# Kernel optimization log

Hardware: AMD Instinct MI355X
Metric: run time of the kernel (lower is better)

## Reference

```python
import jax, jax.numpy as jnp
import numpy as np

DIM, HEADS, HEAD_DIM = 1024, 16, 64
B, L, S = 4, 2048, 2048
EPS = 1e-5
NEG_INF = -1e9


def rms_norm(x, w):
    # x: [..., d]; normalize over last dim, scale by learned weight w [d]
    var = jnp.mean(jnp.square(x), axis=-1, keepdims=True)
    return x * jax.lax.rsqrt(var + EPS) * w


def setup_inputs() -> dict:
    key = jax.random.key(0)
    ks = jax.random.split(key, 9)
    hd = HEADS * HEAD_DIM
    scale = 1.0 / np.sqrt(DIM)
    return {
        "q": jax.random.normal(ks[0], (B, L, DIM), dtype=jnp.float32),
        "kv": jax.random.normal(ks[1], (B, S, DIM), dtype=jnp.float32),
        "x_seqlens": jax.random.randint(ks[2], (B,), 1, S + 1, dtype=jnp.int32),
        "Wq": jax.random.normal(ks[3], (DIM, hd), dtype=jnp.float32) * scale,
        "Wk": jax.random.normal(ks[4], (DIM, hd), dtype=jnp.float32) * scale,
        "Wv": jax.random.normal(ks[5], (DIM, hd), dtype=jnp.float32) * scale,
        "Wo": jax.random.normal(ks[6], (hd, DIM), dtype=jnp.float32) * (1.0 / np.sqrt(hd)),
        "q_norm_w": jnp.ones((HEAD_DIM,), dtype=jnp.float32),
        "k_norm_w": jnp.ones((HEAD_DIM,), dtype=jnp.float32),
    }


def reference(q, kv, x_seqlens, Wq, Wk, Wv, Wo, q_norm_w, k_norm_w):
    b, l, _ = q.shape
    s = kv.shape[1]
    # QKV projections -> [b, h, n, d]
    qh = (q @ Wq).reshape(b, l, HEADS, HEAD_DIM).transpose(0, 2, 1, 3)
    kh = (kv @ Wk).reshape(b, s, HEADS, HEAD_DIM).transpose(0, 2, 1, 3)
    vh = (kv @ Wv).reshape(b, s, HEADS, HEAD_DIM).transpose(0, 2, 1, 3)
    # per-head RMSNorm on q and k
    qh = rms_norm(qh, q_norm_w)
    kh = rms_norm(kh, k_norm_w)
    # dense padding mask [b, 1, 1, s]: True where kv position is valid
    mask = (jnp.arange(s, dtype=jnp.int32)[None, :] < x_seqlens[:, None])[:, None, None, :]
    # scaled dot-product attention (math path: full score matrix)
    scores = jnp.einsum("bhld,bhsd->bhls", qh, kh) * (1.0 / np.sqrt(HEAD_DIM))
    scores = jnp.where(mask, scores, NEG_INF)
    attn = jax.nn.softmax(scores, axis=-1)
    o = jnp.einsum("bhls,bhsd->bhld", attn, vh)  # [b, h, l, d]
    o = o.transpose(0, 2, 1, 3).reshape(b, l, HEADS * HEAD_DIM)
    return o @ Wo
```

## Files before the change

### kernel.cpp

```cpp
#include <hip/hip_runtime.h>
#include <hip/hip_bf16.h>
#include <stdint.h>

#define BB 4
#define LL 2048
#define SS 2048
#define DIMM 1024
#define HH 16
#define HD 64
#define NHD 1024

typedef __bf16 bf16_t;
typedef __bf16 bf16x8 __attribute__((ext_vector_type(8)));
typedef __bf16 bf16x4 __attribute__((ext_vector_type(4)));
typedef float f32x4 __attribute__((ext_vector_type(4)));

#define GLDS16(g, l) __builtin_amdgcn_global_load_lds( \
    (const __attribute__((address_space(1))) void*)(g), \
    (__attribute__((address_space(3))) void*)(l), 16, 0, 0)

#define FENCED_BARRIER() do {                    \
    asm volatile("" ::: "memory");               \
    __builtin_amdgcn_s_barrier();                \
    asm volatile("" ::: "memory");               \
    __builtin_amdgcn_sched_barrier(0);           \
  } while (0)

__global__ __launch_bounds__(256) void cvt_bf16(const float* __restrict__ in,
                                                bf16_t* __restrict__ out) {
  size_t i = (size_t)(blockIdx.x * 256 + threadIdx.x) * 8;
  const f32x4* p = (const f32x4*)(in + i);
  f32x4 a = p[0], b = p[1];
  bf16x8 o;
#pragma unroll
  for (int j = 0; j < 4; ++j) { o[j] = (bf16_t)a[j]; o[4 + j] = (bf16_t)b[j]; }
  *(bf16x8*)(out + i) = o;
}

__global__ __launch_bounds__(256) void transpose_cvt(const float* __restrict__ in,
                                                     bf16_t* __restrict__ out) {
  __shared__ float tile[64][65];
  const int r0 = blockIdx.y * 64, c0 = blockIdx.x * 64;
  const int tr = threadIdx.x >> 2;
  const int tc4 = (threadIdx.x & 3) * 16;
#pragma unroll
  for (int i = 0; i < 4; ++i) {
    f32x4 v = *(const f32x4*)&in[(size_t)(r0 + tr) * 1024 + c0 + tc4 + i * 4];
    tile[tr][tc4 + i * 4 + 0] = v.x;
    tile[tr][tc4 + i * 4 + 1] = v.y;
    tile[tr][tc4 + i * 4 + 2] = v.z;
    tile[tr][tc4 + i * 4 + 3] = v.w;
  }
  __syncthreads();
#pragma unroll
  for (int i = 0; i < 2; ++i) {
    bf16x8 o;
#pragma unroll
    for (int j = 0; j < 8; ++j) o[j] = (bf16_t)tile[tc4 + i * 8 + j][tr];
    *(bf16x8*)&out[(size_t)(c0 + tr) * 1024 + r0 + tc4 + i * 8] = o;
  }
}

template <int NORM, int OUTMODE>
__global__ __launch_bounds__(256) void gemm128(const bf16_t* __restrict__ A,
                                               const bf16_t* __restrict__ Bt,
                                               void* __restrict__ Cout,
                                               const float* __restrict__ normw,
                                               float postscale,
                                               int M, int N, int K) {
  __shared__ bf16_t As[2][4096];
  __shared__ bf16_t Bs[2][4096];
  const int tid = threadIdx.x, lane = tid & 63, w = tid >> 6;
  const int m0 = blockIdx.y * 128, n0 = blockIdx.x * 128;
  const int wm = (w >> 1) * 64, wn = (w & 1) * 64;
  const int fr = lane & 15, fg = lane >> 4;
  f32x4 acc[4][4] = {};
  const int nkt = K >> 5;

  auto stage = [&](int kt, int bi) {
    const int kb = kt * 32;
#pragma unroll
    for (int j = 0; j < 2; ++j) {
      int e = (j * 4 + w) * 512 + lane * 8;
      int r = e >> 5, c = e & 31;
      GLDS16(A  + (size_t)(m0 + r) * K + kb + c, &As[bi][(j * 4 + w) * 512]);
      GLDS16(Bt + (size_t)(n0 + r) * K + kb + c, &Bs[bi][(j * 4 + w) * 512]);
    }
  };

  stage(0, 0);
  int cur = 0;
  for (int kt = 0; kt < nkt; ++kt) {
    if (kt + 1 < nkt) {
      stage(kt + 1, cur ^ 1);
      asm volatile("s_waitcnt vmcnt(4)" ::: "memory");
    } else {
      asm volatile("s_waitcnt vmcnt(0)" ::: "memory");
    }
    FENCED_BARRIER();
    bf16x8 a[4], b[4];
#pragma unroll
    for (int m = 0; m < 4; ++m) a[m] = *(const bf16x8*)&As[cur][(wm + m * 16 + fr) * 32 + fg * 8];
#pragma unroll
    for (int n = 0; n < 4; ++n) b[n] = *(const bf16x8*)&Bs[cur][(wn + n * 16 + fr) * 32 + fg * 8];
    __builtin_amdgcn_s_setprio(1);
#pragma unroll
    for (int m = 0; m < 4; ++m)
#pragma unroll
      for (int n = 0; n < 4; ++n)
        acc[m][n] = __builtin_amdgcn_mfma_f32_16x16x32_bf16(a[m], b[n], acc[m][n], 0, 0, 0);
    __builtin_amdgcn_s_setprio(0);
    FENCED_BARRIER();
    cur ^= 1;
  }
  float w4[4];
  if (NORM) {
#pragma unroll
    for (int n = 0; n < 4; ++n) w4[n] = normw[n * 16 + fr] * postscale;
  }
#pragma unroll
  for (int m = 0; m < 4; ++m) {
    if (NORM) {
      float ss[4];
#pragma unroll
      for (int j = 0; j < 4; ++j) {
        ss[j] = 0.f;
#pragma unroll
        for (int n = 0; n < 4; ++n) ss[j] += acc[m][n][j] * acc[m][n][j];
      }
#pragma unroll
      for (int d = 1; d < 16; d <<= 1)
#pragma unroll
        for (int j = 0; j < 4; ++j) ss[j] += __shfl_xor(ss[j], d);
      float rs[4];
#pragma unroll
      for (int j = 0; j < 4; ++j) rs[j] = rsqrtf(ss[j] * (1.f / 64.f) + 1e-5f);
#pragma unroll
      for (int n = 0; n < 4; ++n)
#pragma unroll
        for (int j = 0; j < 4; ++j) acc[m][n][j] *= rs[j] * w4[n];
    }
    if (OUTMODE == 2) {
      int r = m0 + wm + m * 16 + fg * 4;
      int bb_ = r >> 11, s0 = r & 2047;
#pragma unroll
      for (int n = 0; n < 4; ++n) {
        int cc = n0 + wn + n * 16 + fr;
        int hh_ = cc >> 6, dd = cc & 63;
        bf16x4 pk;
#pragma unroll
        for (int j = 0; j < 4; ++j) pk[j] = (bf16_t)acc[m][n][j];
        *(bf16x4*)&((bf16_t*)Cout)[(((size_t)bb_ * 16 + hh_) * 64 + dd) * 2048 + s0] = pk;
      }
    } else {
#pragma unroll
      for (int n = 0; n < 4; ++n)
#pragma unroll
        for (int j = 0; j < 4; ++j) {
          size_t row = (size_t)m0 + wm + m * 16 + fg * 4 + j;
          size_t col = (size_t)n0 + wn + n * 16 + fr;
          if (OUTMODE == 1)
            ((float*)Cout)[row * N + col] = acc[m][n][j];
          else
            ((bf16_t*)Cout)[row * N + col] = (bf16_t)acc[m][n][j];
        }
    }
  }
}

__global__ __launch_bounds__(256, 3) void attn64(const bf16_t* __restrict__ Qb,
                                                 const bf16_t* __restrict__ Kb,
                                                 const bf16_t* __restrict__ Vtg,
                                                 bf16_t* __restrict__ Ob,
                                                 const int* __restrict__ seqlens) {
  __shared__ bf16_t Kl[2][4096];
  __shared__ bf16_t Vl[2][4096];
  __shared__ bf16_t Pl[8192];
  const int tid = threadIdx.x, lane = tid & 63, w = tid >> 6;
  const int fr = lane & 15, fg = lane >> 4;
  const int qt = blockIdx.x, bh = blockIdx.y;
  const int b = bh >> 4, h = bh & 15;
  const int seqlen = seqlens[b];
  const int ntiles = (seqlen + 63) >> 6;
  bf16_t* Pw = &Pl[w * 2048];

  const bf16_t* qp = Qb + ((size_t)b * LL + qt * 128 + w * 32 + fr) * NHD + h * 64;
  bf16x8 qf[2][2];
#pragma unroll
  for (int qs = 0; qs < 2; ++qs) {
    qf[qs][0] = *(const bf16x8*)&qp[(size_t)qs * 16 * NHD + fg * 8];
    qf[qs][1] = *(const bf16x8*)&qp[(size_t)qs * 16 * NHD + 32 + fg * 8];
  }
  asm volatile("s_waitcnt vmcnt(0)" ::: "memory");

  const bf16_t* Kg = Kb + (size_t)b * SS * NHD + h * 64;
  const bf16_t* Vg = Vtg + ((size_t)(b * 16 + h)) * 64 * SS;

  auto stage = [&](int t, int bi) {
#pragma unroll
    for (int c = 0; c < 2; ++c) {
      const int ro = (w * 2 + c) * 8 + (lane >> 3);
      const int cs = ((lane & 7) ^ (ro & 7)) * 8;
      GLDS16(Kg + (size_t)(t * 64 + ro) * NHD + cs, &Kl[bi][(w * 2 + c) * 512]);
      GLDS16(Vg + (size_t)ro * SS + t * 64 + cs, &Vl[bi][(w * 2 + c) * 512]);
    }
  };

  bf16x8 vones;
#pragma unroll
  for (int i = 0; i < 8; ++i) vones[i] = (bf16_t)1.0f;

  f32x4 oacc[2][4] = {};
  f32x4 lacc[2] = {};
  const float M0 = 12.0f;

  auto softmax_strip = [&](f32x4 (&s)[4], int qs, int t) {
    if (t == ntiles - 1 && (seqlen & 63)) {
#pragma unroll
      for (int n = 0; n < 4; ++n) {
        bool valid = (t * 64 + n * 16 + fr) < seqlen;
#pragma unroll
        for (int j = 0; j < 4; ++j) s[n][j] = valid ? s[n][j] : -1e30f;
      }
    }
#pragma unroll
    for (int n = 0; n < 4; ++n)
#pragma unroll
      for (int j = 0; j < 4; ++j) s[n][j] = __builtin_exp2f(s[n][j] - M0);
#pragma unroll
    for (int n = 0; n < 4; ++n)
#pragma unroll
      for (int j = 0; j < 4; ++j) {
        const int prow = qs * 16 + fg * 4 + j;
        const int pcol = n * 16 + fr;
        Pw[prow * 64 + (((pcol >> 3) ^ (prow & 7)) * 8) + (pcol & 7)] =
            (bf16_t)s[n][j];
      }
  };

  stage(0, 0);
  int cur = 0;
  for (int t = 0; t < ntiles; ++t) {
    if (t + 1 < ntiles) {
      stage(t + 1, cur ^ 1);
      asm volatile("s_waitcnt vmcnt(4)" ::: "memory");
    } else {
      asm volatile("s_waitcnt vmcnt(0)" ::: "memory");
    }
    FENCED_BARRIER();

    f32x4 s0[4] = {}, s1[4] = {};
    __builtin_amdgcn_s_setprio(1);
#pragma unroll
    for (int n = 0; n < 4; ++n) {
      const int rr = n * 16 + fr;
      bf16x8 kf0 = *(const bf16x8*)&Kl[cur][rr * 64 + ((fg ^ (rr & 7)) * 8)];
      bf16x8 kf1 = *(const bf16x8*)&Kl[cur][rr * 64 + (((fg + 4) ^ (rr & 7)) * 8)];
      s0[n] = __builtin_amdgcn_mfma_f32_16x16x32_bf16(qf[0][0], kf0, s0[n], 0, 0, 0);
      s0[n] = __builtin_amdgcn_mfma_f32_16x16x32_bf16(qf[0][1], kf1, s0[n], 0, 0, 0);
      s1[n] = __builtin_amdgcn_mfma_f32_16x16x32_bf16(qf[1][0], kf0, s1[n], 0, 0, 0);
      s1[n] = __builtin_amdgcn_mfma_f32_16x16x32_bf16(qf[1][1], kf1, s1[n], 0, 0, 0);
    }
    __builtin_amdgcn_s_setprio(0);

    softmax_strip(s0, 0, t);
    softmax_strip(s1, 1, t);

    asm volatile("s_waitcnt lgkmcnt(0)" ::: "memory");
    __builtin_amdgcn_sched_barrier(0);

    __builtin_amdgcn_s_setprio(1);
#pragma unroll
    for (int ks = 0; ks < 2; ++ks) {
      const int pr0 = fr, pr1 = 16 + fr;
      bf16x8 pa0 = *(const bf16x8*)&Pw[pr0 * 64 + (((ks * 4 + fg) ^ (pr0 & 7)) * 8)];
      bf16x8 pa1 = *(const bf16x8*)&Pw[pr1 * 64 + (((ks * 4 + fg) ^ (pr1 & 7)) * 8)];
#pragma unroll
      for (int n = 0; n < 4; ++n) {
        const int rr = n * 16 + fr;
        bf16x8 vf = *(const bf16x8*)&Vl[cur][rr * 64 + (((ks * 4 + fg) ^ (rr & 7)) * 8)];
        oacc[0][n] = __builtin_amdgcn_mfma_f32_16x16x32_bf16(pa0, vf, oacc[0][n], 0, 0, 0);
        oacc[1][n] = __builtin_amdgcn_mfma_f32_16x16x32_bf16(pa1, vf, oacc[1][n], 0, 0, 0);
      }
      lacc[0] = __builtin_amdgcn_mfma_f32_16x16x32_bf16(pa0, vones, lacc[0], 0, 0, 0);
      lacc[1] = __builtin_amdgcn_mfma_f32_16x16x32_bf16(pa1, vones, lacc[1], 0, 0, 0);
    }
    __builtin_amdgcn_s_setprio(0);
    FENCED_BARRIER();
    cur ^= 1;
  }

#pragma unroll
  for (int qs = 0; qs < 2; ++qs) {
    float inv[4];
#pragma unroll
    for (int j = 0; j < 4; ++j) inv[j] = __builtin_amdgcn_rcpf(lacc[qs][j]);
#pragma unroll
    for (int n = 0; n < 4; ++n)
#pragma unroll
      for (int j = 0; j < 4; ++j) {
        size_t row = (size_t)b * LL + qt * 128 + w * 32 + qs * 16 + fg * 4 + j;
        Ob[row * NHD + h * 64 + n * 16 + fr] = (bf16_t)(oacc[qs][n][j] * inv[j]);
      }
  }
}

extern "C" void kernel_launch(void* const* d_in, const int* in_sizes, int n_in,
                              void* d_out, int out_size, void* d_ws, size_t ws_size,
                              hipStream_t stream) {
  const float* q   = (const float*)d_in[0];
  const float* kv  = (const float*)d_in[1];
  const int* seqlens = (const int*)d_in[2];
  const float* Wq = (const float*)d_in[3];
  const float* Wk = (const float*)d_in[4];
  const float* Wv = (const float*)d_in[5];
  const float* Wo = (const float*)d_in[6];
  const float* qw = (const float*)d_in[7];
  const float* kw = (const float*)d_in[8];

  char* ws = (char*)d_ws;
  const size_t MB = 1 << 20;
  bf16_t* Aq  = (bf16_t*)(ws + 0 * MB);
  bf16_t* Akv = (bf16_t*)(ws + 16 * MB);
  bf16_t* WqT = (bf16_t*)(ws + 32 * MB);
  bf16_t* WkT = (bf16_t*)(ws + 34 * MB);
  bf16_t* WvT = (bf16_t*)(ws + 36 * MB);
  bf16_t* WoT = (bf16_t*)(ws + 38 * MB);
  bf16_t* Qb  = (bf16_t*)(ws + 40 * MB);
  bf16_t* Kb  = (bf16_t*)(ws + 56 * MB);
  bf16_t* Vt  = (bf16_t*)(ws + 72 * MB);

  const float QSCALE = 0.125f * 1.44269504088896f;

  cvt_bf16<<<4096, 256, 0, stream>>>(q, Aq);
  cvt_bf16<<<4096, 256, 0, stream>>>(kv, Akv);
  dim3 tg(16, 16);
  transpose_cvt<<<tg, 256, 0, stream>>>(Wq, WqT);
  transpose_cvt<<<tg, 256, 0, stream>>>(Wk, WkT);
  transpose_cvt<<<tg, 256, 0, stream>>>(Wv, WvT);
  transpose_cvt<<<tg, 256, 0, stream>>>(Wo, WoT);
  dim3 gg(1024 / 128, 8192 / 128);
  gemm128<1, 0><<<gg, 256, 0, stream>>>(Aq,  WqT, Qb, qw, QSCALE, 8192, 1024, 1024);
  gemm128<1, 0><<<gg, 256, 0, stream>>>(Akv, WkT, Kb, kw, 1.0f,   8192, 1024, 1024);
  gemm128<0, 2><<<gg, 256, 0, stream>>>(Akv, WvT, Vt, nullptr, 1.0f, 8192, 1024, 1024);
  dim3 ag(LL / 128, BB * HH);
  attn64<<<ag, 256, 0, stream>>>(Qb, Kb, Vt, Aq, seqlens);
  gemm128<0, 1><<<gg, 256, 0, stream>>>(Aq, WoT, d_out, nullptr, 1.0f, 8192, 1024, 1024);
}
```

Baseline: 219.1 us.

## Merge conversion, transpose and QKV projection launches; reorder attention grid

The two input conversions become one launch, as do the four weight transposes. The three Q/K/V projection GEMMs become a single kernel that picks its operands and epilogue from blockIdx.x. This cuts launch count from 11 to 5 and lets the projection blocks fill the GPU together in one wave set, removing tail effects between back-to-back kernels. The attention grid is also swapped so the batch-head index is the fast dimension, which changes block scheduling order and may affect K/V cache reuse.

After: 220.0 us. Within noise of the previous version (+0.4%).

```diff
diff --git a/kernel.cpp b/kernel.cpp
--- a/kernel.cpp
+++ b/kernel.cpp
@@ -26,9 +26,14 @@
     __builtin_amdgcn_sched_barrier(0);           \
   } while (0)
 
-__global__ __launch_bounds__(256) void cvt_bf16(const float* __restrict__ in,
-                                                bf16_t* __restrict__ out) {
-  size_t i = (size_t)(blockIdx.x * 256 + threadIdx.x) * 8;
+__global__ __launch_bounds__(256) void cvt_all(const float* __restrict__ q,
+                                               const float* __restrict__ kv,
+                                               bf16_t* __restrict__ Aq,
+                                               bf16_t* __restrict__ Akv) {
+  const int bi = blockIdx.x;
+  const float* in = (bi < 4096) ? q : kv;
+  bf16_t* out = (bi < 4096) ? Aq : Akv;
+  size_t i = ((size_t)(bi & 4095) * 256 + threadIdx.x) * 8;
   const f32x4* p = (const f32x4*)(in + i);
   f32x4 a = p[0], b = p[1];
   bf16x8 o;
@@ -37,8 +42,15 @@
   *(bf16x8*)(out + i) = o;
 }
 
-__global__ __launch_bounds__(256) void transpose_cvt(const float* __restrict__ in,
-                                                     bf16_t* __restrict__ out) {
+__global__ __launch_bounds__(256) void transpose_all(
+    const float* __restrict__ W0, const float* __restrict__ W1,
+    const float* __restrict__ W2, const float* __restrict__ W3,
+    bf16_t* __restrict__ O0, bf16_t* __restrict__ O1,
+    bf16_t* __restrict__ O2, bf16_t* __restrict__ O3) {
+  const float* in = (blockIdx.z == 0) ? W0 : (blockIdx.z == 1) ? W1
+                    : (blockIdx.z == 2) ? W2 : W3;
+  bf16_t* out = (blockIdx.z == 0) ? O0 : (blockIdx.z == 1) ? O1
+                : (blockIdx.z == 2) ? O2 : O3;
   __shared__ float tile[64][65];
   const int r0 = blockIdx.y * 64, c0 = blockIdx.x * 64;
   const int tr = threadIdx.x >> 2;
@@ -61,21 +73,124 @@
   }
 }
 
-template <int NORM, int OUTMODE>
-__global__ __launch_bounds__(256) void gemm128(const bf16_t* __restrict__ A,
-                                               const bf16_t* __restrict__ Bt,
-                                               void* __restrict__ Cout,
-                                               const float* __restrict__ normw,
-                                               float postscale,
-                                               int M, int N, int K) {
+__global__ __launch_bounds__(256) void proj_qkv(
+    const bf16_t* __restrict__ Aq, const bf16_t* __restrict__ Akv,
+    const bf16_t* __restrict__ WqT, const bf16_t* __restrict__ WkT,
+    const bf16_t* __restrict__ WvT,
+    bf16_t* __restrict__ Qb, bf16_t* __restrict__ Kb, bf16_t* __restrict__ Vt,
+    const float* __restrict__ qw, const float* __restrict__ kw, float qscale) {
   __shared__ bf16_t As[2][4096];
   __shared__ bf16_t Bs[2][4096];
+  const int nt = blockIdx.x;
+  const int mode = (nt < 8) ? 0 : (nt < 16 ? 1 : 2);
+  const bf16_t* A  = (mode == 0) ? Aq : Akv;
+  const bf16_t* Bt = (mode == 0) ? WqT : (mode == 1 ? WkT : WvT);
+  const int n0 = (nt & 7) * 128;
+  const int m0 = blockIdx.y * 128;
+  const int K = 1024;
+  const int tid = threadIdx.x, lane = tid & 63, w = tid >> 6;
+  const int wm = (w >> 1) * 64, wn = (w & 1) * 64;
+  const int fr = lane & 15, fg = lane >> 4;
+  f32x4 acc[4][4] = {};
+
+  auto stage = [&](int kt, int bi) {
+    const int kb = kt * 32;
+#pragma unroll
+    for (int j = 0; j < 2; ++j) {
+      int e = (j * 4 + w) * 512 + lane * 8;
+      int r = e >> 5, c = e & 31;
+      GLDS16(A  + (size_t)(m0 + r) * K + kb + c, &As[bi][(j * 4 + w) * 512]);
+      GLDS16(Bt + (size_t)(n0 + r) * K + kb + c, &Bs[bi][(j * 4 + w) * 512]);
+    }
+  };
+
+  stage(0, 0);
+  int cur = 0;
+  for (int kt = 0; kt < 32; ++kt) {
+    if (kt + 1 < 32) {
+      stage(kt + 1, cur ^ 1);
+      asm volatile("s_waitcnt vmcnt(4)" ::: "memory");
+    } else {
+      asm volatile("s_waitcnt vmcnt(0)" ::: "memory");
+    }
+    FENCED_BARRIER();
+    bf16x8 a[4], b[4];
+#pragma unroll
+    for (int m = 0; m < 4; ++m) a[m] = *(const bf16x8*)&As[cur][(wm + m * 16 + fr) * 32 + fg * 8];
+#pragma unroll
+    for (int n = 0; n < 4; ++n) b[n] = *(const bf16x8*)&Bs[cur][(wn + n * 16 + fr) * 32 + fg * 8];
+    __builtin_amdgcn_s_setprio(1);
+#pragma unroll
+    for (int m = 0; m < 4; ++m)
+#pragma unroll
+      for (int n = 0; n < 4; ++n)
+        acc[m][n] = __builtin_amdgcn_mfma_f32_16x16x32_bf16(a[m], b[n], acc[m][n], 0, 0, 0);
+    __builtin_amdgcn_s_setprio(0);
+    FENCED_BARRIER();
+    cur ^= 1;
+  }
+
+  if (mode <= 1) {
+    const float* nw = (mode == 0) ? qw : kw;
+    const float ps = (mode == 0) ? qscale : 1.0f;
+    bf16_t* Cb = (mode == 0) ? Qb : Kb;
+    float w4[4];
+#pragma unroll
+    for (int n = 0; n < 4; ++n) w4[n] = nw[n * 16 + fr] * ps;
+#pragma unroll
+    for (int m = 0; m < 4; ++m) {
+      float ss[4];
+#pragma unroll
+      for (int j = 0; j < 4; ++j) {
+        ss[j] = 0.f;
+#pragma unroll
+        for (int n = 0; n < 4; ++n) ss[j] += acc[m][n][j] * acc[m][n][j];
+      }
+#pragma unroll
+      for (int d = 1; d < 16; d <<= 1)
+#pragma unroll
+        for (int j = 0; j < 4; ++j) ss[j] += __shfl_xor(ss[j], d);
+      float rs[4];
+#pragma unroll
+      for (int j = 0; j < 4; ++j) rs[j] = rsqrtf(ss[j] * (1.f / 64.f) + 1e-5f);
+#pragma unroll
+      for (int n = 0; n < 4; ++n)
+#pragma unroll
+        for (int j = 0; j < 4; ++j) {
+          size_t row = (size_t)m0 + wm + m * 16 + fg * 4 + j;
+          size_t col = (size_t)n0 + wn + n * 16 + fr;
+          Cb[row * NHD + col] = (bf16_t)(acc[m][n][j] * rs[j] * w4[n]);
+        }
+    }
+  } else {
+#pragma unroll
+    for (int m = 0; m < 4; ++m) {
+      int r = m0 + wm + m * 16 + fg * 4;
+      int bb_ = r >> 11, s0 = r & 2047;
+#pragma unroll
+      for (int n = 0; n < 4; ++n) {
+        int cc = n0 + wn + n * 16 + fr;
+        int hh_ = cc >> 6, dd = cc & 63;
+        bf16x4 pk;
+#pragma unroll
+        for (int j = 0; j < 4; ++j) pk[j] = (bf16_t)acc[m][n][j];
+        *(bf16x4*)&Vt[(((size_t)bb_ * 16 + hh_) * 64 + dd) * 2048 + s0] = pk;
+      }
+    }
+  }
+}
+
+__global__ __launch_bounds__(256) void gemm_out(const bf16_t* __restrict__ A,
+                                                const bf16_t* __restrict__ Bt,
+                                                float* __restrict__ Cout) {
+  __shared__ bf16_t As[2][4096];
+  __shared__ bf16_t Bs[2][4096];
+  const int K = 1024, N = 1024;
   const int tid = threadIdx.x, lane = tid & 63, w = tid >> 6;
   const int m0 = blockIdx.y * 128, n0 = blockIdx.x * 128;
   const int wm = (w >> 1) * 64, wn = (w & 1) * 64;
   const int fr = lane & 15, fg = lane >> 4;
   f32x4 acc[4][4] = {};
-  const int nkt = K >> 5;
 
   auto stage = [&](int kt, int bi) {
     const int kb = kt * 32;
@@ -90,8 +205,8 @@
 
   stage(0, 0);
   int cur = 0;
-  for (int kt = 0; kt < nkt; ++kt) {
-    if (kt + 1 < nkt) {
+  for (int kt = 0; kt < 32; ++kt) {
+    if (kt + 1 < 32) {
       stage(kt + 1, cur ^ 1);
       asm volatile("s_waitcnt vmcnt(4)" ::: "memory");
     } else {
@@ -113,59 +228,16 @@
     FENCED_BARRIER();
     cur ^= 1;
   }
-  float w4[4];
-  if (NORM) {
-#pragma unroll
-    for (int n = 0; n < 4; ++n) w4[n] = normw[n * 16 + fr] * postscale;
-  }
-#pragma unroll
-  for (int m = 0; m < 4; ++m) {
-    if (NORM) {
-      float ss[4];
+#pragma unroll
+  for (int m = 0; m < 4; ++m)
+#pragma unroll
+    for (int n = 0; n < 4; ++n)
 #pragma unroll
       for (int j = 0; j < 4; ++j) {
-        ss[j] = 0.f;
-#pragma unroll
-        for (int n = 0; n < 4; ++n) ss[j] += acc[m][n][j] * acc[m][n][j];
-      }
-#pragma unroll
-      for (int d = 1; d < 16; d <<= 1)
-#pragma unroll
-        for (int j = 0; j < 4; ++j) ss[j] += __shfl_xor(ss[j], d);
-      float rs[4];
-#pragma unroll
-      for (int j = 0; j < 4; ++j) rs[j] = rsqrtf(ss[j] * (1.f / 64.f) + 1e-5f);
-#pragma unroll
-      for (int n = 0; n < 4; ++n)
-#pragma unroll
-        for (int j = 0; j < 4; ++j) acc[m][n][j] *= rs[j] * w4[n];
-    }
-    if (OUTMODE == 2) {
-      int r = m0 + wm + m * 16 + fg * 4;
-      int bb_ = r >> 11, s0 = r & 2047;
-#pragma unroll
-      for (int n = 0; n < 4; ++n) {
-        int cc = n0 + wn + n * 16 + fr;
-        int hh_ = cc >> 6, dd = cc & 63;
-        bf16x4 pk;
-#pragma unroll
-        for (int j = 0; j < 4; ++j) pk[j] = (bf16_t)acc[m][n][j];
-        *(bf16x4*)&((bf16_t*)Cout)[(((size_t)bb_ * 16 + hh_) * 64 + dd) * 2048 + s0] = pk;
-      }
-    } else {
-#pragma unroll
-      for (int n = 0; n < 4; ++n)
-#pragma unroll
-        for (int j = 0; j < 4; ++j) {
-          size_t row = (size_t)m0 + wm + m * 16 + fg * 4 + j;
-          size_t col = (size_t)n0 + wn + n * 16 + fr;
-          if (OUTMODE == 1)
-            ((float*)Cout)[row * N + col] = acc[m][n][j];
-          else
-            ((bf16_t*)Cout)[row * N + col] = (bf16_t)acc[m][n][j];
-        }
-    }
-  }
+        size_t row = (size_t)m0 + wm + m * 16 + fg * 4 + j;
+        size_t col = (size_t)n0 + wn + n * 16 + fr;
+        Cout[row * N + col] = acc[m][n][j];
+      }
 }
 
 __global__ __launch_bounds__(256, 3) void attn64(const bf16_t* __restrict__ Qb,
@@ -178,7 +250,7 @@
   __shared__ bf16_t Pl[8192];
   const int tid = threadIdx.x, lane = tid & 63, w = tid >> 6;
   const int fr = lane & 15, fg = lane >> 4;
-  const int qt = blockIdx.x, bh = blockIdx.y;
+  const int qt = blockIdx.y, bh = blockIdx.x;
   const int b = bh >> 4, h = bh & 15;
   const int seqlen = seqlens[b];
   const int ntiles = (seqlen + 63) >> 6;
@@ -332,18 +404,14 @@
 
   const float QSCALE = 0.125f * 1.44269504088896f;
 
-  cvt_bf16<<<4096, 256, 0, stream>>>(q, Aq);
-  cvt_bf16<<<4096, 256, 0, stream>>>(kv, Akv);
-  dim3 tg(16, 16);
-  transpose_cvt<<<tg, 256, 0, stream>>>(Wq, WqT);
-  transpose_cvt<<<tg, 256, 0, stream>>>(Wk, WkT);
-  transpose_cvt<<<tg, 256, 0, stream>>>(Wv, WvT);
-  transpose_cvt<<<tg, 256, 0, stream>>>(Wo, WoT);
-  dim3 gg(1024 / 128, 8192 / 128);
-  gemm128<1, 0><<<gg, 256, 0, stream>>>(Aq,  WqT, Qb, qw, QSCALE, 8192, 1024, 1024);
-  gemm128<1, 0><<<gg, 256, 0, stream>>>(Akv, WkT, Kb, kw, 1.0f,   8192, 1024, 1024);
-  gemm128<0, 2><<<gg, 256, 0, stream>>>(Akv, WvT, Vt, nullptr, 1.0f, 8192, 1024, 1024);
-  dim3 ag(LL / 128, BB * HH);
+  cvt_all<<<8192, 256, 0, stream>>>(q, kv, Aq, Akv);
+  dim3 tg(16, 16, 4);
+  transpose_all<<<tg, 256, 0, stream>>>(Wq, Wk, Wv, Wo, WqT, WkT, WvT, WoT);
+  dim3 pg(24, 64);
+  proj_qkv<<<pg, 256, 0, stream>>>(Aq, Akv, WqT, WkT, WvT, Qb, Kb, Vt,
+                                   qw, kw, QSCALE);
+  dim3 ag(BB * HH, LL / 128);
   attn64<<<ag, 256, 0, stream>>>(Qb, Kb, Vt, Aq, seqlens);
-  gemm128<0, 1><<<gg, 256, 0, stream>>>(Aq, WoT, d_out, nullptr, 1.0f, 8192, 1024, 1024);
-}
+  dim3 og(8, 64);
+  gemm_out<<<og, 256, 0, stream>>>(Aq, WoT, (float*)d_out);
+}
```
